# Kernel tuning notes

Measured on AMD Instinct MI355X. Metric: run time of the kernel, lower is better.

## Reference

```python
import jax, jax.numpy as jnp
import numpy as np

B, L, E, H = 128, 256, 512, 512
S = 0.05  # weight scale


def setup_inputs() -> dict:
    key = jax.random.key(0)
    ks = jax.random.split(key, 12)
    return {
        "embedded_inputs": jax.random.normal(ks[0], (B, L, E), jnp.float32),
        "decoder_input": jax.random.normal(ks[1], (B, E), jnp.float32),
        "h0": jax.random.normal(ks[2], (B, H), jnp.float32),
        "c0": jax.random.normal(ks[3], (B, H), jnp.float32),
        "context": jax.random.normal(ks[4], (B, L, H), jnp.float32),
        "Wih": jax.random.normal(ks[5], (4 * H, E), jnp.float32) * S,
        "bih": jnp.zeros((4 * H,), jnp.float32),
        "Whh": jax.random.normal(ks[6], (4 * H, H), jnp.float32) * S,
        "bhh": jnp.zeros((4 * H,), jnp.float32),
        "Who": jax.random.normal(ks[7], (H, 2 * H), jnp.float32) * S,
        "bho": jnp.zeros((H,), jnp.float32),
        "Wa_in": jax.random.normal(ks[8], (H, H), jnp.float32) * S,
        "ba_in": jnp.zeros((H,), jnp.float32),
        "Wa_ctx": jax.random.normal(ks[9], (H, H), jnp.float32) * S,  # Conv1d(H,H,1) == per-position linear
        "ba_ctx": jnp.zeros((H,), jnp.float32),
        "V": jax.random.uniform(ks[10], (H,), jnp.float32, -1.0, 1.0),
    }


def reference(embedded_inputs, decoder_input, h0, c0, context,
              Wih, bih, Whh, bhh, Who, bho,
              Wa_in, ba_in, Wa_ctx, ba_ctx, V):
    Bsz, Ln, Ed = embedded_inputs.shape
    # context_linear (1x1 conv) depends only on context: precompute ctx [B,H,L]
    ctx = jnp.einsum('blh,oh->bol', context, Wa_ctx) + ba_ctx[None, :, None]
    mask0 = jnp.ones((Bsz, Ln), dtype=embedded_inputs.dtype)

    def step(carry, _):
        h, c, mask, dec_in = carry
        # LSTM cell gates
        gates = dec_in @ Wih.T + bih + h @ Whh.T + bhh  # [B,4H]
        ig, fg, gg, og = jnp.split(gates, 4, axis=1)
        c_t = jax.nn.sigmoid(fg) * c + jax.nn.sigmoid(ig) * jnp.tanh(gg)
        h_lstm = jax.nn.sigmoid(og) * jnp.tanh(c_t)
        # additive attention
        inp = h_lstm @ Wa_in.T + ba_in                     # [B,H]
        att = jnp.einsum('h,bhl->bl', V, jnp.tanh(inp[:, :, None] + ctx))
        att = jnp.where(mask == 0, -jnp.inf, att)
        alpha = jax.nn.softmax(att, axis=1)                # [B,L]
        hs = jnp.einsum('bhl,bl->bh', ctx, alpha)          # attention readout
        h_t = jnp.tanh(jnp.concatenate([hs, h_lstm], axis=1) @ Who.T + bho)
        # pointer selection + mask update
        idx = jnp.argmax(alpha * mask, axis=1)             # [B]
        onehot = jax.nn.one_hot(idx, Ln, dtype=mask.dtype)
        new_mask = mask * (1.0 - onehot)
        dec_next = jnp.take_along_axis(embedded_inputs, idx[:, None, None], axis=1)[:, 0, :]
        return (h_t, c_t, new_mask, dec_next), (alpha, idx)

    (hF, cF, _, _), (alphas, idxs) = jax.lax.scan(
        step, (h0, c0, mask0, decoder_input), None, length=Ln)
    outputs = jnp.transpose(alphas, (1, 0, 2))   # [B,L,L]
    pointers = jnp.transpose(idxs, (1, 0))       # [B,L]
    return outputs, pointers, hF, cF
```

## Files before the change

### kernel.cpp

```cpp
#include <hip/hip_runtime.h>
#include <math.h>

namespace {
constexpr int Bn = 128, Ln = 256, En = 512, Hn = 512;

constexpr long WS_CTX  = 1024;
constexpr long WS_H    = WS_CTX + (long)Bn * Ln * Hn;
constexpr long WS_C    = WS_H   + (long)Bn * Hn;
constexpr long WS_HL   = WS_C   + (long)Bn * Hn;
constexpr long WS_INP  = WS_HL  + (long)Bn * Hn;
constexpr long WS_HS   = WS_INP + (long)Bn * Hn;
constexpr long WS_DEC  = WS_HS  + (long)Bn * Hn;
constexpr long WS_ATT  = WS_DEC + (long)Bn * En;
constexpr long WS_MASK = WS_ATT + (long)Bn * Ln;

constexpr long OUT_PTR = (long)Bn * Ln * Ln;
constexpr long OUT_HF  = OUT_PTR + (long)Bn * Ln;
constexpr long OUT_CF  = OUT_HF + (long)Bn * Hn;
}

struct PParams {
  const float *emb, *dec0, *h0, *c0;
  const float *Wih, *bih, *Whh, *bhh;
  const float *Who, *bho, *Wa_in, *ba_in, *V;
  float *ws, *out;
};

__device__ __forceinline__ void gsync(unsigned* ub, unsigned target, int blk) {
  __syncthreads();
  if (threadIdx.x == 0) {
    unsigned* shard  = ub + (blk & 3) * 64;
    unsigned* master = ub + 512;
    unsigned* gen    = ub + 576;
    bool released = false;
    unsigned n = __hip_atomic_fetch_add(shard, 1u, __ATOMIC_ACQ_REL, __HIP_MEMORY_SCOPE_AGENT);
    if (n == 63u) {
      __hip_atomic_store(shard, 0u, __ATOMIC_RELAXED, __HIP_MEMORY_SCOPE_AGENT);
      unsigned mn = __hip_atomic_fetch_add(master, 1u, __ATOMIC_ACQ_REL, __HIP_MEMORY_SCOPE_AGENT);
      if (mn == 3u) {
        __hip_atomic_store(master, 0u, __ATOMIC_RELAXED, __HIP_MEMORY_SCOPE_AGENT);
        __hip_atomic_store(gen, target, __ATOMIC_RELEASE, __HIP_MEMORY_SCOPE_AGENT);
        released = true;
      }
    }
    if (!released) {
      while (__hip_atomic_load(gen, __ATOMIC_RELAXED, __HIP_MEMORY_SCOPE_AGENT) < target)
        __builtin_amdgcn_s_sleep(2);
      (void)__hip_atomic_load(gen, __ATOMIC_ACQUIRE, __HIP_MEMORY_SCOPE_AGENT);
    }
  }
  __syncthreads();
}

__device__ __forceinline__ void stage_tile(float4* __restrict__ Xs, const float* __restrict__ src,
                                           int bt, int koff, int tid) {
  const int r  = tid >> 5;
  const int ks = tid & 31;
  const float4* g = (const float4*)(src + (size_t)(bt * 32 + r) * 512 + koff);
#pragma unroll
  for (int u = 0; u < 2; ++u) {
    int k4 = ks * 2 + u;
    Xs[r * 64 + (k4 ^ (r & 7))] = g[k4];
  }
}

__launch_bounds__(256)
__global__ void ctx_precompute(const float* __restrict__ context,
                               const float* __restrict__ Wa,
                               const float* __restrict__ ba,
                               float* __restrict__ ws) {
  __shared__ __align__(16) float As[16 * 68];
  __shared__ __align__(16) float Wsm[16 * 68];
  float* ctx = ws + WS_CTX;
  const int mt = blockIdx.x >> 3;
  const int nt = blockIdx.x & 7;
  const int t = threadIdx.x;
  const int tm = t & 15, tn = t >> 4;
  float acc00=0,acc01=0,acc02=0,acc03=0, acc10=0,acc11=0,acc12=0,acc13=0;
  float acc20=0,acc21=0,acc22=0,acc23=0, acc30=0,acc31=0,acc32=0,acc33=0;

  for (int kt = 0; kt < 32; ++kt) {
    __syncthreads();
    {
      const int m = t >> 2, k4 = t & 3;
      float4 a = *(const float4*)(context + (size_t)(mt * 64 + m) * 512 + kt * 16 + k4 * 4);
      As[(k4*4+0)*68 + m] = a.x; As[(k4*4+1)*68 + m] = a.y;
      As[(k4*4+2)*68 + m] = a.z; As[(k4*4+3)*68 + m] = a.w;
      float4 w = *(const float4*)(Wa + (size_t)(nt * 64 + m) * 512 + kt * 16 + k4 * 4);
      Wsm[(k4*4+0)*68 + m] = w.x; Wsm[(k4*4+1)*68 + m] = w.y;
      Wsm[(k4*4+2)*68 + m] = w.z; Wsm[(k4*4+3)*68 + m] = w.w;
    }
    __syncthreads();
#pragma unroll
    for (int k = 0; k < 16; ++k) {
      float4 a4 = *(const float4*)(As + k * 68 + tm * 4);
      float4 b4 = *(const float4*)(Wsm + k * 68 + tn * 4);
      acc00 = fmaf(a4.x, b4.x, acc00); acc01 = fmaf(a4.x, b4.y, acc01);
      acc02 = fmaf(a4.x, b4.z, acc02); acc03 = fmaf(a4.x, b4.w, acc03);
      acc10 = fmaf(a4.y, b4.x, acc10); acc11 = fmaf(a4.y, b4.y, acc11);
      acc12 = fmaf(a4.y, b4.z, acc12); acc13 = fmaf(a4.y, b4.w, acc13);
      acc20 = fmaf(a4.z, b4.x, acc20); acc21 = fmaf(a4.z, b4.y, acc21);
      acc22 = fmaf(a4.z, b4.z, acc22); acc23 = fmaf(a4.z, b4.w, acc23);
      acc30 = fmaf(a4.w, b4.x, acc30); acc31 = fmaf(a4.w, b4.y, acc31);
      acc32 = fmaf(a4.w, b4.z, acc32); acc33 = fmaf(a4.w, b4.w, acc33);
    }
  }
  const int col = nt * 64 + tn * 4;
  float4 bias = *(const float4*)(ba + col);
  float4 o0 = {acc00 + bias.x, acc01 + bias.y, acc02 + bias.z, acc03 + bias.w};
  float4 o1 = {acc10 + bias.x, acc11 + bias.y, acc12 + bias.z, acc13 + bias.w};
  float4 o2 = {acc20 + bias.x, acc21 + bias.y, acc22 + bias.z, acc23 + bias.w};
  float4 o3 = {acc30 + bias.x, acc31 + bias.y, acc32 + bias.z, acc33 + bias.w};
  const size_t base = (size_t)(mt * 64 + tm * 4) * 512 + col;
  *(float4*)(ctx + base + 0 * 512) = o0;
  *(float4*)(ctx + base + 1 * 512) = o1;
  *(float4*)(ctx + base + 2 * 512) = o2;
  *(float4*)(ctx + base + 3 * 512) = o3;
}

__launch_bounds__(1024, 4)
__global__ void pdecoder_main(PParams p) {
  __shared__ __align__(16) float smem[8192];
  float4* Xs = (float4*)smem;

  float* ws = p.ws;
  unsigned* ub = (unsigned*)ws;
  unsigned tgt = 0;
  const int t = threadIdx.x, blk = blockIdx.x;

  float* ctx    = ws + WS_CTX;
  float* hbuf   = ws + WS_H;
  float* cbuf   = ws + WS_C;
  float* hlbuf  = ws + WS_HL;
  float* inpbuf = ws + WS_INP;
  float* hsbuf  = ws + WS_HS;
  float* decbuf = ws + WS_DEC;
  float* attbuf = ws + WS_ATT;
  float* maskbuf= ws + WS_MASK;

  {
    int idx = blk * 1024 + t;
    if (idx < Bn * Hn) { hbuf[idx] = p.h0[idx]; cbuf[idx] = p.c0[idx]; }
    if (idx < Bn * En) decbuf[idx] = p.dec0[idx];
    if (idx < Bn * Ln) maskbuf[idx] = 1.0f;
  }
  gsync(ub, ++tgt, blk);

  for (int step = 0; step < Ln; ++step) {
    {
      const int bt = blk >> 6, ht = blk & 63;
      const int bi = t & 31, cg = t >> 5;
      const int j0 = cg & 7, g = cg >> 3;
      const int gc = g * 512 + ht * 8 + j0;
      float acc = 0.f;
#pragma unroll
      for (int kt = 0; kt < 4; ++kt) {
        __syncthreads();
        stage_tile(Xs, (kt < 2) ? decbuf : hbuf, bt, (kt & 1) * 256, t);
        __syncthreads();
        const float4* W4 = (const float4*)(((kt < 2) ? p.Wih : p.Whh) + (size_t)gc * 512 + (kt & 1) * 256);
#pragma unroll 4
        for (int k4 = 0; k4 < 64; ++k4) {
          float4 x = Xs[bi * 64 + (k4 ^ (bi & 7))];
          float4 w = W4[k4];
          acc = fmaf(x.x, w.x, acc); acc = fmaf(x.y, w.y, acc);
          acc = fmaf(x.z, w.z, acc); acc = fmaf(x.w, w.w, acc);
        }
      }
      __syncthreads();
      float* gs = smem;
      gs[bi * 33 + cg] = acc + p.bih[gc] + p.bhh[gc];
      __syncthreads();
      if (t < 256) {
        const int j = t & 7, bi2 = t >> 3;
        float ig = gs[bi2 * 33 + j];
        float fg = gs[bi2 * 33 + 8 + j];
        float gg = gs[bi2 * 33 + 16 + j];
        float og = gs[bi2 * 33 + 24 + j];
        const int b = bt * 32 + bi2, h = ht * 8 + j;
        float cold = cbuf[b * 512 + h];
        float is = 1.f / (1.f + expf(-ig));
        float fs = 1.f / (1.f + expf(-fg));
        float os = 1.f / (1.f + expf(-og));
        float ct = fs * cold + is * tanhf(gg);
        float hl = os * tanhf(ct);
        cbuf[b * 512 + h] = ct;
        hlbuf[b * 512 + h] = hl;
      }
    }
    gsync(ub, ++tgt, blk);

    {
      const int bt = blk >> 6, ot = blk & 63;
      const int bi = t & 31, oj = t >> 5;
      float acc = 0.f;
#pragma unroll
      for (int kt = 0; kt < 2; ++kt) {
        __syncthreads();
        stage_tile(Xs, hlbuf, bt, kt * 256, t);
        __syncthreads();
        if (t < 256) {
          const float4* Wr = (const float4*)(p.Wa_in + (size_t)(ot * 8 + oj) * 512 + kt * 256);
#pragma unroll 4
          for (int k4 = 0; k4 < 64; ++k4) {
            float4 x = Xs[bi * 64 + (k4 ^ (bi & 7))];
            float4 w = Wr[k4];
            acc = fmaf(x.x, w.x, acc); acc = fmaf(x.y, w.y, acc);
            acc = fmaf(x.z, w.z, acc); acc = fmaf(x.w, w.w, acc);
          }
        }
      }
      if (t < 256) {
        const int o = ot * 8 + oj;
        inpbuf[(bt * 32 + bi) * 512 + o] = acc + p.ba_in[o];
      }
    }
    gsync(ub, ++tgt, blk);

    {
      const int b = blk >> 1, ph = blk & 1;
      float* inp_s = smem;
      float* V_s   = smem + 512;
      if (t < 512) { inp_s[t] = inpbuf[b * 512 + t]; V_s[t] = p.V[t]; }
      __syncthreads();
      const int w = t >> 6, lane = t & 63;
      const float4* inp4 = (const float4*)inp_s;
      const float4* V4   = (const float4*)V_s;
      float4 i0 = inp4[lane],  i1 = inp4[64 + lane];
      float4 v0 = V4[lane],    v1 = V4[64 + lane];
      for (int i = 0; i < 8; ++i) {
        const int l = ph * 128 + w * 8 + i;
        float msk = maskbuf[b * 256 + l];
        if (msk == 0.f) {
          if (lane == 0) attbuf[b * 256 + l] = -INFINITY;
          continue;
        }
        const float4* row = (const float4*)(ctx + (size_t)(b * 256 + l) * 512);
        float4 c0 = row[lane], c1 = row[64 + lane];
        float a;
        a = v0.x * tanhf(i0.x + c0.x);
        a = fmaf(v0.y, tanhf(i0.y + c0.y), a);
        a = fmaf(v0.z, tanhf(i0.z + c0.z), a);
        a = fmaf(v0.w, tanhf(i0.w + c0.w), a);
        a = fmaf(v1.x, tanhf(i1.x + c1.x), a);
        a = fmaf(v1.y, tanhf(i1.y + c1.y), a);
        a = fmaf(v1.z, tanhf(i1.z + c1.z), a);
        a = fmaf(v1.w, tanhf(i1.w + c1.w), a);
#pragma unroll
        for (int off = 32; off > 0; off >>= 1) a += __shfl_xor(a, off, 64);
        if (lane == 0) attbuf[b * 256 + l] = a;
      }
    }
    gsync(ub, ++tgt, blk);

    {
      const int b = blk >> 1, ph = blk & 1;
      float* att_s   = smem;
      float* val_s   = smem + 256;
      int*   idx_s   = (int*)(smem + 512);
      float* alpha_s = smem + 768;
      float* part_s  = smem + 1024;
      if (t < 256) {
        float a = attbuf[b * 256 + t];
        att_s[t] = a; val_s[t] = a; idx_s[t] = t;
      }
      __syncthreads();
      for (int s = 128; s > 0; s >>= 1) {
        if (t < s) {
          float v1 = val_s[t], v2 = val_s[t + s];
          int   i1 = idx_s[t], i2 = idx_s[t + s];
          if (v2 > v1 || (v2 == v1 && i2 < i1)) { val_s[t] = v2; idx_s[t] = i2; }
        }
        __syncthreads();
      }
      const float m = val_s[0];
      const int am = idx_s[0];
      __syncthreads();
      if (t < 256) {
        float e = expf(att_s[t] - m);
        alpha_s[t] = e; val_s[t] = e;
      }
      __syncthreads();
      for (int s = 128; s > 0; s >>= 1) {
        if (t < s) val_s[t] += val_s[t + s];
        __syncthreads();
      }
      const float Z = val_s[0];
      __syncthreads();
      if (t < 256) alpha_s[t] = alpha_s[t] / Z;
      __syncthreads();
      if (ph == 0) {
        if (t < 256) p.out[(size_t)b * Ln * Ln + (size_t)step * Ln + t] = alpha_s[t];
        if (t == 0) {
          p.out[OUT_PTR + (size_t)b * Ln + step] = (float)am;
          maskbuf[b * 256 + am] = 0.f;
        }
        if (t < 512) decbuf[b * 512 + t] = p.emb[((size_t)(b * 256) + am) * 512 + t];
      }
      const int hi = t & 255, lp = (t >> 8) & 1;
      const int h = ph * 256 + hi;
      float acc = 0.f;
      if (t < 512) {
        const float* cb = ctx + (size_t)b * 256 * 512 + h;
#pragma unroll 4
        for (int l = lp * 128; l < lp * 128 + 128; ++l) {
          float al = alpha_s[l];
          if (al != 0.f) acc = fmaf(al, cb[(size_t)l * 512], acc);
        }
      }
      if (t < 512 && lp == 1) part_s[hi] = acc;
      __syncthreads();
      if (t < 512 && lp == 0) hsbuf[(size_t)b * 512 + h] = acc + part_s[hi];
    }
    gsync(ub, ++tgt, blk);

    {
      const int bt = blk >> 6, ot = blk & 63;
      const int bi = t & 31, s = (t >> 5) & 15;
      const int oj = s & 7, kh = s >> 3;
      const int o = ot * 8 + oj;
      float acc = 0.f;
#pragma unroll
      for (int kt = 0; kt < 4; ++kt) {
        __syncthreads();
        stage_tile(Xs, (kt < 2) ? hsbuf : hlbuf, bt, (kt & 1) * 256, t);
        __syncthreads();
        if (t < 512 && (kt >> 1) == kh) {
          const float4* Wr = (const float4*)(p.Who + (size_t)o * 1024 + kt * 256);
#pragma unroll 4
          for (int k4 = 0; k4 < 64; ++k4) {
            float4 x = Xs[bi * 64 + (k4 ^ (bi & 7))];
            float4 w = Wr[k4];
            acc = fmaf(x.x, w.x, acc); acc = fmaf(x.y, w.y, acc);
            acc = fmaf(x.z, w.z, acc); acc = fmaf(x.w, w.w, acc);
          }
        }
      }
      __syncthreads();
      float* part = smem;
      if (t < 512) part[bi * 17 + s] = acc;
      __syncthreads();
      if (t < 256) {
        const int bi2 = t & 31, oj2 = t >> 5;
        float v = part[bi2 * 17 + oj2] + part[bi2 * 17 + 8 + oj2];
        const int o2 = ot * 8 + oj2, bb = bt * 32 + bi2;
        hbuf[bb * 512 + o2] = tanhf(v + p.bho[o2]);
      }
    }
    gsync(ub, ++tgt, blk);
  }

  {
    int idx = blk * 1024 + t;
    if (idx < Bn * Hn) {
      p.out[OUT_HF + idx] = hbuf[idx];
      p.out[OUT_CF + idx] = cbuf[idx];
    }
  }
}

extern "C" void kernel_launch(void* const* d_in, const int* in_sizes, int n_in,
                              void* d_out, int out_size, void* d_ws, size_t ws_size,
                              hipStream_t stream) {
  (void)in_sizes; (void)n_in; (void)out_size; (void)ws_size;
  const float* emb     = (const float*)d_in[0];
  const float* dec0    = (const float*)d_in[1];
  const float* h0      = (const float*)d_in[2];
  const float* c0      = (const float*)d_in[3];
  const float* context = (const float*)d_in[4];
  const float* Wih     = (const float*)d_in[5];
  const float* bih     = (const float*)d_in[6];
  const float* Whh     = (const float*)d_in[7];
  const float* bhh     = (const float*)d_in[8];
  const float* Who     = (const float*)d_in[9];
  const float* bho     = (const float*)d_in[10];
  const float* Wa_in   = (const float*)d_in[11];
  const float* ba_in   = (const float*)d_in[12];
  const float* Wa_ctx  = (const float*)d_in[13];
  const float* ba_ctx  = (const float*)d_in[14];
  const float* V       = (const float*)d_in[15];
  float* ws  = (float*)d_ws;
  float* out = (float*)d_out;

  hipMemsetAsync(d_ws, 0, 4096, stream);

  hipLaunchKernelGGL(ctx_precompute, dim3(4096), dim3(256), 0, stream,
                     context, Wa_ctx, ba_ctx, ws);

  PParams prm{emb, dec0, h0, c0, Wih, bih, Whh, bhh, Who, bho, Wa_in, ba_in, V, ws, out};
  void* args[] = {&prm};
  hipLaunchCooperativeKernel((const void*)pdecoder_main, dim3(256), dim3(1024),
                             args, 0, stream);
}
```

Measured before the change: 43.30 ms.

## Fuse post-LSTM stages into one per-batch block to cut grid barriers

```diff
diff --git a/kernel.cpp b/kernel.cpp
--- a/kernel.cpp
+++ b/kernel.cpp
@@ -8,11 +8,7 @@
 constexpr long WS_H    = WS_CTX + (long)Bn * Ln * Hn;
 constexpr long WS_C    = WS_H   + (long)Bn * Hn;
 constexpr long WS_HL   = WS_C   + (long)Bn * Hn;
-constexpr long WS_INP  = WS_HL  + (long)Bn * Hn;
-constexpr long WS_HS   = WS_INP + (long)Bn * Hn;
-constexpr long WS_DEC  = WS_HS  + (long)Bn * Hn;
-constexpr long WS_ATT  = WS_DEC + (long)Bn * En;
-constexpr long WS_MASK = WS_ATT + (long)Bn * Ln;
+constexpr long WS_DEC  = WS_HL  + (long)Bn * Hn;
 
 constexpr long OUT_PTR = (long)Bn * Ln * Ln;
 constexpr long OUT_HF  = OUT_PTR + (long)Bn * Ln;
@@ -52,18 +48,6 @@
   __syncthreads();
 }
 
-__device__ __forceinline__ void stage_tile(float4* __restrict__ Xs, const float* __restrict__ src,
-                                           int bt, int koff, int tid) {
-  const int r  = tid >> 5;
-  const int ks = tid & 31;
-  const float4* g = (const float4*)(src + (size_t)(bt * 32 + r) * 512 + koff);
-#pragma unroll
-  for (int u = 0; u < 2; ++u) {
-    int k4 = ks * 2 + u;
-    Xs[r * 64 + (k4 ^ (r & 7))] = g[k4];
-  }
-}
-
 __launch_bounds__(256)
 __global__ void ctx_precompute(const float* __restrict__ context,
                                const float* __restrict__ Wa,
@@ -121,7 +105,8 @@
 __launch_bounds__(1024, 4)
 __global__ void pdecoder_main(PParams p) {
   __shared__ __align__(16) float smem[8192];
-  float4* Xs = (float4*)smem;
+  float* V_s    = smem + 7168;
+  float* mask_s = smem + 7680;
 
   float* ws = p.ws;
   unsigned* ub = (unsigned*)ws;
@@ -132,52 +117,58 @@
   float* hbuf   = ws + WS_H;
   float* cbuf   = ws + WS_C;
   float* hlbuf  = ws + WS_HL;
-  float* inpbuf = ws + WS_INP;
-  float* hsbuf  = ws + WS_HS;
   float* decbuf = ws + WS_DEC;
-  float* attbuf = ws + WS_ATT;
-  float* maskbuf= ws + WS_MASK;
 
   {
     int idx = blk * 1024 + t;
     if (idx < Bn * Hn) { hbuf[idx] = p.h0[idx]; cbuf[idx] = p.c0[idx]; }
     if (idx < Bn * En) decbuf[idx] = p.dec0[idx];
-    if (idx < Bn * Ln) maskbuf[idx] = 1.0f;
+  }
+  if (blk < Bn) {
+    if (t < Hn) V_s[t] = p.V[t];
+    if (t < Ln) mask_s[t] = 1.0f;
   }
   gsync(ub, ++tgt, blk);
 
   for (int step = 0; step < Ln; ++step) {
     {
-      const int bt = blk >> 6, ht = blk & 63;
-      const int bi = t & 31, cg = t >> 5;
-      const int j0 = cg & 7, g = cg >> 3;
-      const int gc = g * 512 + ht * 8 + j0;
+      const int bt = blk >> 5, htt = blk & 31;
+      const int bi = t & 15, cg = t >> 4;
+      const int j0 = cg & 15, g = cg >> 4;
+      const int gc = g * 512 + htt * 16 + j0;
+      const int r = t >> 6, ks = t & 63;
+      float4* Xs16 = (float4*)smem;
       float acc = 0.f;
+      float4 pre = ((const float4*)(decbuf + (size_t)(bt * 16 + r) * 512))[ks];
 #pragma unroll
       for (int kt = 0; kt < 4; ++kt) {
         __syncthreads();
-        stage_tile(Xs, (kt < 2) ? decbuf : hbuf, bt, (kt & 1) * 256, t);
-        __syncthreads();
+        Xs16[r * 64 + (ks ^ (r & 7))] = pre;
+        __syncthreads();
+        if (kt < 3) {
+          const float* src = (kt + 1 < 2) ? decbuf : hbuf;
+          pre = ((const float4*)(src + (size_t)(bt * 16 + r) * 512 + ((kt + 1) & 1) * 256))[ks];
+        }
         const float4* W4 = (const float4*)(((kt < 2) ? p.Wih : p.Whh) + (size_t)gc * 512 + (kt & 1) * 256);
-#pragma unroll 4
+#pragma unroll 8
         for (int k4 = 0; k4 < 64; ++k4) {
-          float4 x = Xs[bi * 64 + (k4 ^ (bi & 7))];
+          float4 x = Xs16[bi * 64 + (k4 ^ (bi & 7))];
           float4 w = W4[k4];
           acc = fmaf(x.x, w.x, acc); acc = fmaf(x.y, w.y, acc);
           acc = fmaf(x.z, w.z, acc); acc = fmaf(x.w, w.w, acc);
         }
       }
       __syncthreads();
-      float* gs = smem;
-      gs[bi * 33 + cg] = acc + p.bih[gc] + p.bhh[gc];
+      float* gs = smem + 4096;
+      gs[bi * 65 + cg] = acc + p.bih[gc] + p.bhh[gc];
       __syncthreads();
       if (t < 256) {
-        const int j = t & 7, bi2 = t >> 3;
-        float ig = gs[bi2 * 33 + j];
-        float fg = gs[bi2 * 33 + 8 + j];
-        float gg = gs[bi2 * 33 + 16 + j];
-        float og = gs[bi2 * 33 + 24 + j];
-        const int b = bt * 32 + bi2, h = ht * 8 + j;
+        const int j = t & 15, bi2 = t >> 4;
+        float ig = gs[bi2 * 65 + j];
+        float fg = gs[bi2 * 65 + 16 + j];
+        float gg = gs[bi2 * 65 + 32 + j];
+        float og = gs[bi2 * 65 + 48 + j];
+        const int b = bt * 16 + bi2, h = htt * 16 + j;
         float cold = cbuf[b * 512 + h];
         float is = 1.f / (1.f + expf(-ig));
         float fs = 1.f / (1.f + expf(-fg));
@@ -190,161 +181,134 @@
     }
     gsync(ub, ++tgt, blk);
 
-    {
-      const int bt = blk >> 6, ot = blk & 63;
-      const int bi = t & 31, oj = t >> 5;
-      float acc = 0.f;
+    if (blk < Bn) {
+      const int b = blk;
+      float* hl_s    = smem;
+      float* hs_s    = smem + 512;
+      float* inp_s   = smem + 1024;
+      float* att_s   = smem + 1536;
+      float* val_s   = smem + 1792;
+      int*   idx_s   = (int*)(smem + 2048);
+      float* alpha_s = smem + 2304;
+      float* part2   = smem + 2560;
+      float* partF   = smem + 3072;
+
+      if (t < 128) ((float4*)hl_s)[t] = ((const float4*)(hlbuf + (size_t)b * 512))[t];
+      __syncthreads();
+
+      if (t < 512) {
+        const float4* xv = (const float4*)hl_s;
+        const float4* Wr = (const float4*)(p.Wa_in + (size_t)t * 512);
+        float acc = 0.f;
+#pragma unroll 4
+        for (int k4 = 0; k4 < 128; ++k4) {
+          float4 x = xv[k4], w = Wr[k4];
+          acc = fmaf(x.x, w.x, acc); acc = fmaf(x.y, w.y, acc);
+          acc = fmaf(x.z, w.z, acc); acc = fmaf(x.w, w.w, acc);
+        }
+        inp_s[t] = acc + p.ba_in[t];
+      }
+      __syncthreads();
+
+      {
+        const int wv = t >> 6, lane = t & 63;
+        const float4* inp4 = (const float4*)inp_s;
+        const float4* V4   = (const float4*)V_s;
+        float4 i0 = inp4[lane],  i1 = inp4[64 + lane];
+        float4 v0 = V4[lane],    v1 = V4[64 + lane];
+        const float4* row = (const float4*)(ctx + ((size_t)b * 256 + (size_t)wv * 16) * 512);
+        float4 c0 = row[lane], c1 = row[64 + lane];
+        for (int i = 0; i < 16; ++i) {
+          const int l = wv * 16 + i;
+          float4 cc0 = c0, cc1 = c1;
+          if (i < 15) {
+            const float4* nr = row + (size_t)(i + 1) * 128;
+            c0 = nr[lane]; c1 = nr[64 + lane];
+          }
+          if (mask_s[l] != 0.f) {
+            float a;
+            a = v0.x * tanhf(i0.x + cc0.x);
+            a = fmaf(v0.y, tanhf(i0.y + cc0.y), a);
+            a = fmaf(v0.z, tanhf(i0.z + cc0.z), a);
+            a = fmaf(v0.w, tanhf(i0.w + cc0.w), a);
+            a = fmaf(v1.x, tanhf(i1.x + cc1.x), a);
+            a = fmaf(v1.y, tanhf(i1.y + cc1.y), a);
+            a = fmaf(v1.z, tanhf(i1.z + cc1.z), a);
+            a = fmaf(v1.w, tanhf(i1.w + cc1.w), a);
 #pragma unroll
-      for (int kt = 0; kt < 2; ++kt) {
-        __syncthreads();
-        stage_tile(Xs, hlbuf, bt, kt * 256, t);
+            for (int off = 32; off > 0; off >>= 1) a += __shfl_xor(a, off, 64);
+            if (lane == 0) att_s[l] = a;
+          } else {
+            if (lane == 0) att_s[l] = -INFINITY;
+          }
+        }
+      }
+      __syncthreads();
+
+      {
+        if (t < 256) { float a = att_s[t]; val_s[t] = a; idx_s[t] = t; }
+        __syncthreads();
+        for (int s = 128; s > 0; s >>= 1) {
+          if (t < s) {
+            float v1 = val_s[t], v2 = val_s[t + s];
+            int   i1_ = idx_s[t], i2_ = idx_s[t + s];
+            if (v2 > v1 || (v2 == v1 && i2_ < i1_)) { val_s[t] = v2; idx_s[t] = i2_; }
+          }
+          __syncthreads();
+        }
+        const float m = val_s[0];
+        const int am = idx_s[0];
         __syncthreads();
         if (t < 256) {
-          const float4* Wr = (const float4*)(p.Wa_in + (size_t)(ot * 8 + oj) * 512 + kt * 256);
-#pragma unroll 4
-          for (int k4 = 0; k4 < 64; ++k4) {
-            float4 x = Xs[bi * 64 + (k4 ^ (bi & 7))];
-            float4 w = Wr[k4];
-            acc = fmaf(x.x, w.x, acc); acc = fmaf(x.y, w.y, acc);
-            acc = fmaf(x.z, w.z, acc); acc = fmaf(x.w, w.w, acc);
-          }
-        }
-      }
-      if (t < 256) {
-        const int o = ot * 8 + oj;
-        inpbuf[(bt * 32 + bi) * 512 + o] = acc + p.ba_in[o];
-      }
-    }
-    gsync(ub, ++tgt, blk);
-
-    {
-      const int b = blk >> 1, ph = blk & 1;
-      float* inp_s = smem;
-      float* V_s   = smem + 512;
-      if (t < 512) { inp_s[t] = inpbuf[b * 512 + t]; V_s[t] = p.V[t]; }
-      __syncthreads();
-      const int w = t >> 6, lane = t & 63;
-      const float4* inp4 = (const float4*)inp_s;
-      const float4* V4   = (const float4*)V_s;
-      float4 i0 = inp4[lane],  i1 = inp4[64 + lane];
-      float4 v0 = V4[lane],    v1 = V4[64 + lane];
-      for (int i = 0; i < 8; ++i) {
-        const int l = ph * 128 + w * 8 + i;
-        float msk = maskbuf[b * 256 + l];
-        if (msk == 0.f) {
-          if (lane == 0) attbuf[b * 256 + l] = -INFINITY;
-          continue;
-        }
-        const float4* row = (const float4*)(ctx + (size_t)(b * 256 + l) * 512);
-        float4 c0 = row[lane], c1 = row[64 + lane];
-        float a;
-        a = v0.x * tanhf(i0.x + c0.x);
-        a = fmaf(v0.y, tanhf(i0.y + c0.y), a);
-        a = fmaf(v0.z, tanhf(i0.z + c0.z), a);
-        a = fmaf(v0.w, tanhf(i0.w + c0.w), a);
-        a = fmaf(v1.x, tanhf(i1.x + c1.x), a);
-        a = fmaf(v1.y, tanhf(i1.y + c1.y), a);
-        a = fmaf(v1.z, tanhf(i1.z + c1.z), a);
-        a = fmaf(v1.w, tanhf(i1.w + c1.w), a);
-#pragma unroll
-        for (int off = 32; off > 0; off >>= 1) a += __shfl_xor(a, off, 64);
-        if (lane == 0) attbuf[b * 256 + l] = a;
-      }
-    }
-    gsync(ub, ++tgt, blk);
-
-    {
-      const int b = blk >> 1, ph = blk & 1;
-      float* att_s   = smem;
-      float* val_s   = smem + 256;
-      int*   idx_s   = (int*)(smem + 512);
-      float* alpha_s = smem + 768;
-      float* part_s  = smem + 1024;
-      if (t < 256) {
-        float a = attbuf[b * 256 + t];
-        att_s[t] = a; val_s[t] = a; idx_s[t] = t;
-      }
-      __syncthreads();
-      for (int s = 128; s > 0; s >>= 1) {
-        if (t < s) {
-          float v1 = val_s[t], v2 = val_s[t + s];
-          int   i1 = idx_s[t], i2 = idx_s[t + s];
-          if (v2 > v1 || (v2 == v1 && i2 < i1)) { val_s[t] = v2; idx_s[t] = i2; }
-        }
-        __syncthreads();
-      }
-      const float m = val_s[0];
-      const int am = idx_s[0];
-      __syncthreads();
-      if (t < 256) {
-        float e = expf(att_s[t] - m);
-        alpha_s[t] = e; val_s[t] = e;
-      }
-      __syncthreads();
-      for (int s = 128; s > 0; s >>= 1) {
-        if (t < s) val_s[t] += val_s[t + s];
-        __syncthreads();
-      }
-      const float Z = val_s[0];
-      __syncthreads();
-      if (t < 256) alpha_s[t] = alpha_s[t] / Z;
-      __syncthreads();
-      if (ph == 0) {
+          float e = expf(att_s[t] - m);
+          alpha_s[t] = e; val_s[t] = e;
+        }
+        __syncthreads();
+        for (int s = 128; s > 0; s >>= 1) {
+          if (t < s) val_s[t] += val_s[t + s];
+          __syncthreads();
+        }
+        const float Z = val_s[0];
+        __syncthreads();
+        if (t < 256) alpha_s[t] = alpha_s[t] / Z;
+        __syncthreads();
         if (t < 256) p.out[(size_t)b * Ln * Ln + (size_t)step * Ln + t] = alpha_s[t];
         if (t == 0) {
           p.out[OUT_PTR + (size_t)b * Ln + step] = (float)am;
-          maskbuf[b * 256 + am] = 0.f;
+          mask_s[am] = 0.f;
         }
         if (t < 512) decbuf[b * 512 + t] = p.emb[((size_t)(b * 256) + am) * 512 + t];
-      }
-      const int hi = t & 255, lp = (t >> 8) & 1;
-      const int h = ph * 256 + hi;
-      float acc = 0.f;
-      if (t < 512) {
-        const float* cb = ctx + (size_t)b * 256 * 512 + h;
+        const int hi = t & 255, lp = (t >> 8) & 1, ph2 = t >> 9;
+        const int h = ph2 * 256 + hi;
+        float acc = 0.f;
+        {
+          const float* cb = ctx + (size_t)b * 256 * 512 + h;
 #pragma unroll 4
-        for (int l = lp * 128; l < lp * 128 + 128; ++l) {
-          float al = alpha_s[l];
-          if (al != 0.f) acc = fmaf(al, cb[(size_t)l * 512], acc);
-        }
-      }
-      if (t < 512 && lp == 1) part_s[hi] = acc;
-      __syncthreads();
-      if (t < 512 && lp == 0) hsbuf[(size_t)b * 512 + h] = acc + part_s[hi];
-    }
-    gsync(ub, ++tgt, blk);
-
-    {
-      const int bt = blk >> 6, ot = blk & 63;
-      const int bi = t & 31, s = (t >> 5) & 15;
-      const int oj = s & 7, kh = s >> 3;
-      const int o = ot * 8 + oj;
-      float acc = 0.f;
-#pragma unroll
-      for (int kt = 0; kt < 4; ++kt) {
-        __syncthreads();
-        stage_tile(Xs, (kt < 2) ? hsbuf : hlbuf, bt, (kt & 1) * 256, t);
-        __syncthreads();
-        if (t < 512 && (kt >> 1) == kh) {
-          const float4* Wr = (const float4*)(p.Who + (size_t)o * 1024 + kt * 256);
-#pragma unroll 4
-          for (int k4 = 0; k4 < 64; ++k4) {
-            float4 x = Xs[bi * 64 + (k4 ^ (bi & 7))];
-            float4 w = Wr[k4];
-            acc = fmaf(x.x, w.x, acc); acc = fmaf(x.y, w.y, acc);
-            acc = fmaf(x.z, w.z, acc); acc = fmaf(x.w, w.w, acc);
+          for (int l = lp * 128; l < lp * 128 + 128; ++l) {
+            float al = alpha_s[l];
+            if (al != 0.f) acc = fmaf(al, cb[(size_t)l * 512], acc);
           }
         }
-      }
-      __syncthreads();
-      float* part = smem;
-      if (t < 512) part[bi * 17 + s] = acc;
-      __syncthreads();
-      if (t < 256) {
-        const int bi2 = t & 31, oj2 = t >> 5;
-        float v = part[bi2 * 17 + oj2] + part[bi2 * 17 + 8 + oj2];
-        const int o2 = ot * 8 + oj2, bb = bt * 32 + bi2;
-        hbuf[bb * 512 + o2] = tanhf(v + p.bho[o2]);
+        if (lp == 1) part2[h] = acc;
+        __syncthreads();
+        if (lp == 0) hs_s[h] = acc + part2[h];
+      }
+      __syncthreads();
+
+      {
+        const int o = t & 511, kh = t >> 9;
+        const float4* xv = (const float4*)(kh ? hl_s : hs_s);
+        const float4* Wr = (const float4*)(p.Who + (size_t)o * 1024 + (size_t)kh * 512);
+        float acc = 0.f;
+#pragma unroll 8
+        for (int k4 = 0; k4 < 128; ++k4) {
+          float4 x = xv[k4], w = Wr[k4];
+          acc = fmaf(x.x, w.x, acc); acc = fmaf(x.y, w.y, acc);
+          acc = fmaf(x.z, w.z, acc); acc = fmaf(x.w, w.w, acc);
+        }
+        if (kh == 1) partF[o] = acc;
+        __syncthreads();
+        if (kh == 0) hbuf[(size_t)b * 512 + o] = tanhf(acc + partF[o] + p.bho[o]);
       }
     }
     gsync(ub, ++tgt, blk);
```

After: 46.54 ms. +7.5%, slower.

## Replace sharded barrier with flag-gather barrier and re-tile decoder GEMM phases

Applied to the files above, without the earlier changes.

```diff
diff --git a/kernel.cpp b/kernel.cpp
--- a/kernel.cpp
+++ b/kernel.cpp
@@ -4,7 +4,7 @@
 namespace {
 constexpr int Bn = 128, Ln = 256, En = 512, Hn = 512;
 
-constexpr long WS_CTX  = 1024;
+constexpr long WS_CTX  = 8192;
 constexpr long WS_H    = WS_CTX + (long)Bn * Ln * Hn;
 constexpr long WS_C    = WS_H   + (long)Bn * Hn;
 constexpr long WS_HL   = WS_C   + (long)Bn * Hn;
@@ -28,40 +28,30 @@
 
 __device__ __forceinline__ void gsync(unsigned* ub, unsigned target, int blk) {
   __syncthreads();
-  if (threadIdx.x == 0) {
-    unsigned* shard  = ub + (blk & 3) * 64;
-    unsigned* master = ub + 512;
-    unsigned* gen    = ub + 576;
-    bool released = false;
-    unsigned n = __hip_atomic_fetch_add(shard, 1u, __ATOMIC_ACQ_REL, __HIP_MEMORY_SCOPE_AGENT);
-    if (n == 63u) {
-      __hip_atomic_store(shard, 0u, __ATOMIC_RELAXED, __HIP_MEMORY_SCOPE_AGENT);
-      unsigned mn = __hip_atomic_fetch_add(master, 1u, __ATOMIC_ACQ_REL, __HIP_MEMORY_SCOPE_AGENT);
-      if (mn == 3u) {
-        __hip_atomic_store(master, 0u, __ATOMIC_RELAXED, __HIP_MEMORY_SCOPE_AGENT);
-        __hip_atomic_store(gen, target, __ATOMIC_RELEASE, __HIP_MEMORY_SCOPE_AGENT);
-        released = true;
-      }
-    }
-    if (!released) {
+  unsigned* flags = ub;
+  unsigned* gen   = ub + 4096;
+  const int t = threadIdx.x;
+  if (blk == 0) {
+    for (;;) {
+      unsigned v = (t > 0 && t < 256)
+          ? __hip_atomic_load(&flags[t * 16], __ATOMIC_RELAXED, __HIP_MEMORY_SCOPE_AGENT)
+          : target;
+      int cnt = __syncthreads_count((int)(v >= target));
+      if (cnt == (int)blockDim.x) break;
+      __builtin_amdgcn_s_sleep(2);
+    }
+    __builtin_amdgcn_fence(__ATOMIC_ACQUIRE, "agent");
+    if (t == 0)
+      __hip_atomic_store(gen, target, __ATOMIC_RELEASE, __HIP_MEMORY_SCOPE_AGENT);
+  } else {
+    if (t == 0) {
+      __hip_atomic_store(&flags[blk * 16], target, __ATOMIC_RELEASE, __HIP_MEMORY_SCOPE_AGENT);
       while (__hip_atomic_load(gen, __ATOMIC_RELAXED, __HIP_MEMORY_SCOPE_AGENT) < target)
         __builtin_amdgcn_s_sleep(2);
       (void)__hip_atomic_load(gen, __ATOMIC_ACQUIRE, __HIP_MEMORY_SCOPE_AGENT);
     }
   }
   __syncthreads();
-}
-
-__device__ __forceinline__ void stage_tile(float4* __restrict__ Xs, const float* __restrict__ src,
-                                           int bt, int koff, int tid) {
-  const int r  = tid >> 5;
-  const int ks = tid & 31;
-  const float4* g = (const float4*)(src + (size_t)(bt * 32 + r) * 512 + koff);
-#pragma unroll
-  for (int u = 0; u < 2; ++u) {
-    int k4 = ks * 2 + u;
-    Xs[r * 64 + (k4 ^ (r & 7))] = g[k4];
-  }
 }
 
 __launch_bounds__(256)
@@ -121,7 +111,6 @@
 __launch_bounds__(1024, 4)
 __global__ void pdecoder_main(PParams p) {
   __shared__ __align__(16) float smem[8192];
-  float4* Xs = (float4*)smem;
 
   float* ws = p.ws;
   unsigned* ub = (unsigned*)ws;
@@ -148,36 +137,44 @@
 
   for (int step = 0; step < Ln; ++step) {
     {
-      const int bt = blk >> 6, ht = blk & 63;
-      const int bi = t & 31, cg = t >> 5;
-      const int j0 = cg & 7, g = cg >> 3;
-      const int gc = g * 512 + ht * 8 + j0;
+      const int bt = blk >> 4, gt = blk & 15;
+      const int bi = t & 7, cg = t >> 3;
+      const int j0 = cg & 31, g = cg >> 5;
+      const int gc = g * 512 + gt * 32 + j0;
+      const int r = t >> 6, ks = t & 63;
+      float4* Xs = (float4*)smem;
       float acc = 0.f;
+      float4 pre;
+      if (t < 512) pre = ((const float4*)(decbuf + (size_t)(bt * 8 + r) * 512))[ks];
 #pragma unroll
       for (int kt = 0; kt < 4; ++kt) {
         __syncthreads();
-        stage_tile(Xs, (kt < 2) ? decbuf : hbuf, bt, (kt & 1) * 256, t);
+        if (t < 512) Xs[r * 64 + (ks ^ r)] = pre;
         __syncthreads();
+        if (t < 512 && kt < 3) {
+          const float* src = (kt + 1 < 2) ? decbuf : hbuf;
+          pre = ((const float4*)(src + (size_t)(bt * 8 + r) * 512 + ((kt + 1) & 1) * 256))[ks];
+        }
         const float4* W4 = (const float4*)(((kt < 2) ? p.Wih : p.Whh) + (size_t)gc * 512 + (kt & 1) * 256);
-#pragma unroll 4
+#pragma unroll 8
         for (int k4 = 0; k4 < 64; ++k4) {
-          float4 x = Xs[bi * 64 + (k4 ^ (bi & 7))];
+          float4 x = Xs[bi * 64 + (k4 ^ bi)];
           float4 w = W4[k4];
           acc = fmaf(x.x, w.x, acc); acc = fmaf(x.y, w.y, acc);
           acc = fmaf(x.z, w.z, acc); acc = fmaf(x.w, w.w, acc);
         }
       }
       __syncthreads();
-      float* gs = smem;
-      gs[bi * 33 + cg] = acc + p.bih[gc] + p.bhh[gc];
-      __syncthreads();
-      if (t < 256) {
-        const int j = t & 7, bi2 = t >> 3;
-        float ig = gs[bi2 * 33 + j];
-        float fg = gs[bi2 * 33 + 8 + j];
-        float gg = gs[bi2 * 33 + 16 + j];
-        float og = gs[bi2 * 33 + 24 + j];
-        const int b = bt * 32 + bi2, h = ht * 8 + j;
+      float* gs = smem + 4096;
+      gs[bi * 132 + cg] = acc + p.bih[gc] + p.bhh[gc];
+      __syncthreads();
+      if (t < 256) {
+        const int j = t & 31, bi2 = t >> 5;
+        float ig = gs[bi2 * 132 + j];
+        float fg = gs[bi2 * 132 + 32 + j];
+        float gg = gs[bi2 * 132 + 64 + j];
+        float og = gs[bi2 * 132 + 96 + j];
+        const int b = bt * 8 + bi2, h = gt * 32 + j;
         float cold = cbuf[b * 512 + h];
         float is = 1.f / (1.f + expf(-ig));
         float fs = 1.f / (1.f + expf(-fg));
@@ -191,28 +188,22 @@
     gsync(ub, ++tgt, blk);
 
     {
-      const int bt = blk >> 6, ot = blk & 63;
-      const int bi = t & 31, oj = t >> 5;
-      float acc = 0.f;
-#pragma unroll
-      for (int kt = 0; kt < 2; ++kt) {
-        __syncthreads();
-        stage_tile(Xs, hlbuf, bt, kt * 256, t);
-        __syncthreads();
-        if (t < 256) {
-          const float4* Wr = (const float4*)(p.Wa_in + (size_t)(ot * 8 + oj) * 512 + kt * 256);
+      const int b = blk >> 1, oh = blk & 1;
+      float* hl_s = smem;
+      if (t < 128) ((float4*)hl_s)[t] = ((const float4*)(hlbuf + (size_t)b * 512))[t];
+      __syncthreads();
+      if (t < 256) {
+        const int o = oh * 256 + t;
+        const float4* xv = (const float4*)hl_s;
+        const float4* Wr = (const float4*)(p.Wa_in + (size_t)o * 512);
+        float acc = 0.f;
 #pragma unroll 4
-          for (int k4 = 0; k4 < 64; ++k4) {
-            float4 x = Xs[bi * 64 + (k4 ^ (bi & 7))];
-            float4 w = Wr[k4];
-            acc = fmaf(x.x, w.x, acc); acc = fmaf(x.y, w.y, acc);
-            acc = fmaf(x.z, w.z, acc); acc = fmaf(x.w, w.w, acc);
-          }
-        }
-      }
-      if (t < 256) {
-        const int o = ot * 8 + oj;
-        inpbuf[(bt * 32 + bi) * 512 + o] = acc + p.ba_in[o];
+        for (int k4 = 0; k4 < 128; ++k4) {
+          float4 x = xv[k4], w = Wr[k4];
+          acc = fmaf(x.x, w.x, acc); acc = fmaf(x.y, w.y, acc);
+          acc = fmaf(x.z, w.z, acc); acc = fmaf(x.w, w.w, acc);
+        }
+        inpbuf[b * 512 + o] = acc + p.ba_in[o];
       }
     }
     gsync(ub, ++tgt, blk);
@@ -315,36 +306,33 @@
     gsync(ub, ++tgt, blk);
 
     {
-      const int bt = blk >> 6, ot = blk & 63;
-      const int bi = t & 31, s = (t >> 5) & 15;
-      const int oj = s & 7, kh = s >> 3;
-      const int o = ot * 8 + oj;
+      const int b = blk >> 1, oh = blk & 1;
+      float* hs_s  = smem;
+      float* hl_s  = smem + 512;
+      float* partF = smem + 1024;
+      if (t < 128) {
+        ((float4*)hs_s)[t] = ((const float4*)(hsbuf + (size_t)b * 512))[t];
+        ((float4*)hl_s)[t] = ((const float4*)(hlbuf + (size_t)b * 512))[t];
+      }
+      __syncthreads();
       float acc = 0.f;
-#pragma unroll
-      for (int kt = 0; kt < 4; ++kt) {
-        __syncthreads();
-        stage_tile(Xs, (kt < 2) ? hsbuf : hlbuf, bt, (kt & 1) * 256, t);
-        __syncthreads();
-        if (t < 512 && (kt >> 1) == kh) {
-          const float4* Wr = (const float4*)(p.Who + (size_t)o * 1024 + kt * 256);
+      if (t < 512) {
+        const int oj = t & 255, kh = t >> 8;
+        const int o = oh * 256 + oj;
+        const float4* xv = (const float4*)(kh ? hl_s : hs_s);
+        const float4* Wr = (const float4*)(p.Who + (size_t)o * 1024 + (size_t)kh * 512);
 #pragma unroll 4
-          for (int k4 = 0; k4 < 64; ++k4) {
-            float4 x = Xs[bi * 64 + (k4 ^ (bi & 7))];
-            float4 w = Wr[k4];
-            acc = fmaf(x.x, w.x, acc); acc = fmaf(x.y, w.y, acc);
-            acc = fmaf(x.z, w.z, acc); acc = fmaf(x.w, w.w, acc);
-          }
-        }
-      }
-      __syncthreads();
-      float* part = smem;
-      if (t < 512) part[bi * 17 + s] = acc;
-      __syncthreads();
-      if (t < 256) {
-        const int bi2 = t & 31, oj2 = t >> 5;
-        float v = part[bi2 * 17 + oj2] + part[bi2 * 17 + 8 + oj2];
-        const int o2 = ot * 8 + oj2, bb = bt * 32 + bi2;
-        hbuf[bb * 512 + o2] = tanhf(v + p.bho[o2]);
+        for (int k4 = 0; k4 < 128; ++k4) {
+          float4 x = xv[k4], w = Wr[k4];
+          acc = fmaf(x.x, w.x, acc); acc = fmaf(x.y, w.y, acc);
+          acc = fmaf(x.z, w.z, acc); acc = fmaf(x.w, w.w, acc);
+        }
+        if (kh == 1) partF[oj] = acc;
+      }
+      __syncthreads();
+      if (t < 256) {
+        const int o = oh * 256 + t;
+        hbuf[(size_t)b * 512 + o] = tanhf(acc + partF[t] + p.bho[o]);
       }
     }
     gsync(ub, ++tgt, blk);
@@ -382,7 +370,7 @@
   float* ws  = (float*)d_ws;
   float* out = (float*)d_out;
 
-  hipMemsetAsync(d_ws, 0, 4096, stream);
+  hipMemsetAsync(d_ws, 0, 32768, stream);
 
   hipLaunchKernelGGL(ctx_precompute, dim3(4096), dim3(256), 0, stream,
                      context, Wa_ctx, ba_ctx, ws);
```

After: 43.94 ms. Within noise of the previous version (+1.5%).
